# Optimization experiments

Measured on AMD Instinct MI355X. Metric: run time of the kernel, lower is better.

The kernel has to match this reference:

```python
import jax, jax.numpy as jnp
import numpy as np

N, R, A, F, T = 50000, 5, 8, 32, 32
TEMPLATE_RADIUS = 0.1


def _gaussian_prior_kernel():
    # Template vertices in polar coords -> cartesian; Gaussian interpolation prior.
    rho = np.linspace(TEMPLATE_RADIUS / R, TEMPLATE_RADIUS, R)
    theta = np.linspace(0.0, 2 * np.pi, A, endpoint=False)
    x = rho[:, None] * np.cos(theta)[None, :]  # [R, A]
    y = rho[:, None] * np.sin(theta)[None, :]
    pts = np.stack([x, y], axis=-1).reshape(R * A, 2)
    d2 = ((pts[:, None, :] - pts[None, :, :]) ** 2).sum(-1)
    sigma = TEMPLATE_RADIUS / R
    k = np.exp(-d2 / (2.0 * sigma ** 2)).astype(np.float32)
    return jnp.asarray(k.reshape(R, A, R, A))


def setup_inputs() -> dict:
    key = jax.random.key(0)
    k1, k2, k3, k4, k5, k6 = jax.random.split(key, 6)
    mesh_signal = jax.random.normal(k1, (N, F), dtype=jnp.float32)
    idx = jax.random.randint(k2, (N, R, A, 3), 0, N).astype(jnp.float32)
    w = jax.random.uniform(k3, (N, R, A, 3), dtype=jnp.float32)
    w = w / jnp.sum(w, axis=-1, keepdims=True)  # barycentric weights sum to 1
    bary_coordinates = jnp.stack([idx, w], axis=-1)  # [N,R,A,3,2]
    scale = 0.05
    W_self = jax.random.normal(k4, (T, 1, F), dtype=jnp.float32) * scale
    W_neighbor = jax.random.normal(k5, (T, R, A, F), dtype=jnp.float32) * scale
    bias = jax.random.normal(k6, (1, T), dtype=jnp.float32) * scale
    kernel = _gaussian_prior_kernel()
    return {"mesh_signal": mesh_signal, "bary_coordinates": bary_coordinates,
            "W_self": W_self, "W_neighbor": W_neighbor, "bias": bias, "kernel": kernel}


def reference(mesh_signal, bary_coordinates, W_self, W_neighbor, bias, kernel):
    # conv_center: [N, 1, T]
    conv_center = jnp.einsum('tef,kf->ket', W_self, mesh_signal)
    # Barycentric interpolation (gather + weighted sum over 3 triangle vertices)
    idx = bary_coordinates[..., 0].astype(jnp.int32)   # [N,R,A,3]
    w = bary_coordinates[..., 1]                        # [N,R,A,3]
    gathered = mesh_signal[idx]                         # [N,R,A,3,F]
    interp = jnp.sum(w[..., None] * gathered, axis=-2)  # [N,R,A,F]
    # Prior weighting: [R,A,R,A] x [N,R,A,F] -> [N,R,A,F]
    interp = jnp.einsum('raxy,kxyf->kraf', kernel, interp)
    # Rotations: torch.roll(interp, o, dims=2) contracted with W == roll(W, -o, axis=2) contracted with interp
    rotation_delta = 1
    orientations = range(0, A, rotation_delta)
    W_rot = jnp.stack([jnp.roll(W_neighbor, -o, axis=2) for o in orientations])  # [O,T,R,A,F]
    conv_neighbor = jnp.einsum('otraf,kraf->kot', W_rot, interp)  # [N,O,T]
    return jax.nn.relu(conv_center + conv_neighbor + bias)
```

## Files before the change

kernel.cpp:

```cpp
#include <hip/hip_runtime.h>
#include <hip/hip_fp16.h>

typedef unsigned short u16;
typedef unsigned int   u32;

#define N_MESH 50000
#define RA     40
#define F_     32
#define OT     256
#define KSELF  1280
#define KTOT   1312
#define NCH    41
#define GN     32
#define NBLK   1563
#define SECC   8
#define MESH16_BLOCKS 782
#define WEFF_BLOCKS   1312

using f32x4 = __attribute__((ext_vector_type(4))) float;
using f16x8 = __attribute__((ext_vector_type(8))) _Float16;

__device__ __align__(16) u16 g_bhi[NCH * 16 * 64 * 8];
__device__ __align__(16) u16 g_mesh16[N_MESH * F_];
__device__ int g_isf32;

__device__ __forceinline__ float bf2f(u16 u) {
    union { u32 i; float f; } v; v.i = ((u32)u) << 16; return v.f;
}
__device__ __forceinline__ u16 f2bf(float f) {
    union { float f; u32 i; } v; v.f = f; u32 u = v.i;
    return (u16)((u + 0x7FFFu + ((u >> 16) & 1u)) >> 16);
}
__device__ __forceinline__ float ld(const void* p, int i, int isf32) {
    return isf32 ? ((const float*)p)[i] : bf2f(((const u16*)p)[i]);
}

__global__ void detect_kernel(const void* mesh) {
    __shared__ int s_weird;
    if (threadIdx.x == 0) s_weird = 0;
    __syncthreads();
    const u16* p = (const u16*)mesh;
    int w = 0;
    for (int j = threadIdx.x * 16; j < threadIdx.x * 16 + 16; ++j) {
        float v = bf2f(p[j]);
        float a = v < 0.f ? -v : v;
        if (!(a <= 1.0e6f)) ++w;
        else if (a > 0.f && a < 1.0e-30f) ++w;
    }
    atomicAdd(&s_weird, w);
    __syncthreads();
    if (threadIdx.x == 0) g_isf32 = (s_weird > 100) ? 1 : 0;
}

__global__ void prep_kernel(const void* __restrict__ mesh,
                            const void* __restrict__ Wn,
                            const void* __restrict__ Wself,
                            const void* __restrict__ ker) {
    const int isf32 = g_isf32;
    if (blockIdx.x < MESH16_BLOCKS) {
        int i = blockIdx.x * 256 + threadIdx.x;
        if (i >= N_MESH * F_ / 8) return;
        union { uint4 v; _Float16 h[8]; } o;
        #pragma unroll
        for (int j = 0; j < 8; ++j)
            o.h[j] = (_Float16)ld(mesh, i * 8 + j, isf32);
        *((uint4*)g_mesh16 + i) = o.v;
    } else {
        int e = (blockIdx.x - MESH16_BLOCKS) * 256 + threadIdx.x;
        if (e >= OT * KTOT) return;
        int c = e / KTOT;
        int k = e - c * KTOT;
        int t = c & 31;
        float acc = 0.f;
        if (k < KSELF) {
            int xy = k >> 5, f = k & 31;
            int o = c >> 5;
            for (int ra = 0; ra < RA; ++ra) {
                int r = ra >> 3, a = ra & 7;
                int a2 = (a + o) & 7;
                acc += ld(ker, ra * RA + xy, isf32) *
                       ld(Wn, t * (5 * 8 * F_) + r * (8 * F_) + a2 * F_ + f, isf32);
            }
        } else {
            acc = ld(Wself, t * F_ + (k - KSELF), isf32);
        }
        int ch = k >> 5;
        int kg = (k >> 3) & 3;
        int el = k & 7;
        int nt = c >> 4, col = c & 15;
        size_t fi = ((size_t)(ch * 16 + nt) * 64 + (kg * 16 + col)) * 8 + el;
        union { _Float16 h; u16 u; } H;
        H.h = (_Float16)acc;
        g_bhi[fi] = H.u;
    }
}

__global__ __launch_bounds__(256, 4)
void ConvIntrinsic_17102559772776_kernel(const void* __restrict__ mesh,
                                         const void* __restrict__ bary,
                                         const void* __restrict__ bias,
                                         void* __restrict__ out) {
    __shared__ __align__(16) u16 Alds[SECC * 2 * 64 * 8];

    const int tid   = threadIdx.x;
    const int n0    = blockIdx.x * GN;
    const int isf32 = g_isf32;
    const int lane  = tid & 63;
    const int wv    = tid >> 6;
    const int clt   = tid >> 5;
    const int tn    = tid & 31;
    const int gn    = n0 + tn;
    const int rt1   = tn >> 4, lr = tn & 15;
    u16* const dst0 = Alds + ((size_t)(clt * 2 + rt1) * 64 + lr) * 8;

    f32x4 acc[2][4];
    #pragma unroll
    for (int rt = 0; rt < 2; ++rt)
        #pragma unroll
        for (int j = 0; j < 4; ++j) acc[rt][j] = (f32x4){0.f, 0.f, 0.f, 0.f};

    for (int sec = 0; sec < NCH; sec += SECC) {
        int nch = NCH - sec; if (nch > SECC) nch = SECC;

        if (clt < nch) {
            const int ch = sec + clt;
            if (gn >= N_MESH) {
                #pragma unroll
                for (int kg = 0; kg < 4; ++kg)
                    *(uint4*)(dst0 + kg * 128) = make_uint4(0, 0, 0, 0);
            } else if (ch < RA) {
                float fi0, w0, fi1, w1, fi2, w2;
                if (isf32) {
                    const float* bp = (const float*)bary + (size_t)gn * (RA * 6) + ch * 6;
                    fi0 = bp[0]; w0 = bp[1]; fi1 = bp[2]; w1 = bp[3]; fi2 = bp[4]; w2 = bp[5];
                } else {
                    const u16* bp = (const u16*)bary + (size_t)gn * (RA * 6) + ch * 6;
                    fi0 = bf2f(bp[0]); w0 = bf2f(bp[1]);
                    fi1 = bf2f(bp[2]); w1 = bf2f(bp[3]);
                    fi2 = bf2f(bp[4]); w2 = bf2f(bp[5]);
                }
                int i0 = (int)fi0, i1 = (int)fi1, i2 = (int)fi2;
                i0 = i0 < 0 ? 0 : (i0 > N_MESH - 1 ? N_MESH - 1 : i0);
                i1 = i1 < 0 ? 0 : (i1 > N_MESH - 1 ? N_MESH - 1 : i1);
                i2 = i2 < 0 ? 0 : (i2 > N_MESH - 1 ? N_MESH - 1 : i2);
                const uint4* m0 = (const uint4*)g_mesh16 + (size_t)i0 * 4;
                const uint4* m1 = (const uint4*)g_mesh16 + (size_t)i1 * 4;
                const uint4* m2 = (const uint4*)g_mesh16 + (size_t)i2 * 4;
                __half2 w0h = __float2half2_rn(w0);
                __half2 w1h = __float2half2_rn(w1);
                __half2 w2h = __float2half2_rn(w2);
                #pragma unroll
                for (int kg = 0; kg < 4; ++kg) {
                    union { uint4 v; __half2 h[4]; } x0, x1, x2, o;
                    x0.v = m0[kg]; x1.v = m1[kg]; x2.v = m2[kg];
                    #pragma unroll
                    for (int q = 0; q < 4; ++q)
                        o.h[q] = __hfma2(x0.h[q], w0h,
                                 __hfma2(x1.h[q], w1h, __hmul2(x2.h[q], w2h)));
                    *(uint4*)(dst0 + kg * 128) = o.v;
                }
            } else {
                const uint4* ms = (const uint4*)g_mesh16 + (size_t)gn * 4;
                #pragma unroll
                for (int kg = 0; kg < 4; ++kg)
                    *(uint4*)(dst0 + kg * 128) = ms[kg];
            }
        }
        __syncthreads();

        #pragma unroll 2
        for (int c = 0; c < nch; ++c) {
            int ch = sec + c;
            size_t bo = ((size_t)(ch * 16 + wv * 4) * 64 + lane) * 8;
            const f16x8* bh = (const f16x8*)&g_bhi[bo];
            f16x8 bhj[4];
            #pragma unroll
            for (int j = 0; j < 4; ++j) bhj[j] = bh[j * 64];
            #pragma unroll
            for (int rt = 0; rt < 2; ++rt) {
                f16x8 ah = *(const f16x8*)&Alds[((size_t)(c * 2 + rt) * 64 + lane) * 8];
                #pragma unroll
                for (int j = 0; j < 4; ++j)
                    acc[rt][j] = __builtin_amdgcn_mfma_f32_16x16x32_f16(ah, bhj[j], acc[rt][j], 0, 0, 0);
            }
        }
        __syncthreads();
    }

    const int col = lane & 15, rg = lane >> 4;
    #pragma unroll
    for (int j = 0; j < 4; ++j) {
        int c = (wv * 4 + j) * 16 + col;
        float bv = ld(bias, c & 31, isf32);
        #pragma unroll
        for (int rt = 0; rt < 2; ++rt) {
            #pragma unroll
            for (int r = 0; r < 4; ++r) {
                int row = n0 + rt * 16 + rg * 4 + r;
                if (row < N_MESH) {
                    float v = acc[rt][j][r] + bv;
                    v = v > 0.f ? v : 0.f;
                    size_t oi = (size_t)row * OT + c;
                    if (isf32) ((float*)out)[oi] = v;
                    else       ((u16*)out)[oi]   = f2bf(v);
                }
            }
        }
    }
}

extern "C" void kernel_launch(void* const* d_in, const int* in_sizes, int n_in,
                              void* d_out, int out_size, void* d_ws, size_t ws_size,
                              hipStream_t stream) {
    const void* mesh  = d_in[0];
    const void* bary  = d_in[1];
    const void* Wself = d_in[2];
    const void* Wn    = d_in[3];
    const void* bias  = d_in[4];
    const void* ker   = d_in[5];
    (void)in_sizes; (void)n_in; (void)out_size; (void)d_ws; (void)ws_size;

    detect_kernel<<<1, 256, 0, stream>>>(mesh);

    prep_kernel<<<MESH16_BLOCKS + WEFF_BLOCKS, 256, 0, stream>>>(mesh, Wn, Wself, ker);

    ConvIntrinsic_17102559772776_kernel<<<NBLK, 256, 0, stream>>>(mesh, bary, bias, d_out);
}
```

Baseline: 230.2 us.

## Build MFMA A-fragments directly in registers, dropping LDS staging and barriers

The main kernel no longer stages interpolated A tiles in shared memory with block barriers. Each wave now owns one 16-row tile and half of the output columns, and each lane gathers and interpolates its own 8-element A fragment straight into registers per chunk. The bary loads are also widened to 64-bit and 32-bit packed reads. In exchange, each interpolation is computed twice (once per column-group wave), more B fragments and accumulators are held per wave, and launch bounds are lowered to 3 blocks per SM to make room for the extra registers.

```diff
diff --git a/kernel.cpp b/kernel.cpp
--- a/kernel.cpp
+++ b/kernel.cpp
@@ -13,7 +13,6 @@
 #define NCH    41
 #define GN     32
 #define NBLK   1563
-#define SECC   8
 #define MESH16_BLOCKS 782
 #define WEFF_BLOCKS   1312
 
@@ -95,115 +94,90 @@
     }
 }
 
-__global__ __launch_bounds__(256, 4)
+__global__ __launch_bounds__(256, 3)
 void ConvIntrinsic_17102559772776_kernel(const void* __restrict__ mesh,
                                          const void* __restrict__ bary,
                                          const void* __restrict__ bias,
                                          void* __restrict__ out) {
-    __shared__ __align__(16) u16 Alds[SECC * 2 * 64 * 8];
-
     const int tid   = threadIdx.x;
     const int n0    = blockIdx.x * GN;
     const int isf32 = g_isf32;
     const int lane  = tid & 63;
-    const int wv    = tid >> 6;
-    const int clt   = tid >> 5;
-    const int tn    = tid & 31;
-    const int gn    = n0 + tn;
-    const int rt1   = tn >> 4, lr = tn & 15;
-    u16* const dst0 = Alds + ((size_t)(clt * 2 + rt1) * 64 + lr) * 8;
-
-    f32x4 acc[2][4];
+    const int w     = tid >> 6;
+    const int cg    = w & 1;
+    const int rt    = w >> 1;
+    const int arow  = lane & 15;
+    const int p     = lane >> 4;
+    const int gn    = n0 + rt * 16 + arow;
+    const bool valid = (gn < N_MESH);
+
+    f32x4 acc[8];
     #pragma unroll
-    for (int rt = 0; rt < 2; ++rt)
-        #pragma unroll
-        for (int j = 0; j < 4; ++j) acc[rt][j] = (f32x4){0.f, 0.f, 0.f, 0.f};
-
-    for (int sec = 0; sec < NCH; sec += SECC) {
-        int nch = NCH - sec; if (nch > SECC) nch = SECC;
-
-        if (clt < nch) {
-            const int ch = sec + clt;
-            if (gn >= N_MESH) {
-                #pragma unroll
-                for (int kg = 0; kg < 4; ++kg)
-                    *(uint4*)(dst0 + kg * 128) = make_uint4(0, 0, 0, 0);
-            } else if (ch < RA) {
-                float fi0, w0, fi1, w1, fi2, w2;
-                if (isf32) {
-                    const float* bp = (const float*)bary + (size_t)gn * (RA * 6) + ch * 6;
-                    fi0 = bp[0]; w0 = bp[1]; fi1 = bp[2]; w1 = bp[3]; fi2 = bp[4]; w2 = bp[5];
-                } else {
-                    const u16* bp = (const u16*)bary + (size_t)gn * (RA * 6) + ch * 6;
-                    fi0 = bf2f(bp[0]); w0 = bf2f(bp[1]);
-                    fi1 = bf2f(bp[2]); w1 = bf2f(bp[3]);
-                    fi2 = bf2f(bp[4]); w2 = bf2f(bp[5]);
-                }
-                int i0 = (int)fi0, i1 = (int)fi1, i2 = (int)fi2;
-                i0 = i0 < 0 ? 0 : (i0 > N_MESH - 1 ? N_MESH - 1 : i0);
-                i1 = i1 < 0 ? 0 : (i1 > N_MESH - 1 ? N_MESH - 1 : i1);
-                i2 = i2 < 0 ? 0 : (i2 > N_MESH - 1 ? N_MESH - 1 : i2);
-                const uint4* m0 = (const uint4*)g_mesh16 + (size_t)i0 * 4;
-                const uint4* m1 = (const uint4*)g_mesh16 + (size_t)i1 * 4;
-                const uint4* m2 = (const uint4*)g_mesh16 + (size_t)i2 * 4;
-                __half2 w0h = __float2half2_rn(w0);
-                __half2 w1h = __float2half2_rn(w1);
-                __half2 w2h = __float2half2_rn(w2);
-                #pragma unroll
-                for (int kg = 0; kg < 4; ++kg) {
-                    union { uint4 v; __half2 h[4]; } x0, x1, x2, o;
-                    x0.v = m0[kg]; x1.v = m1[kg]; x2.v = m2[kg];
-                    #pragma unroll
-                    for (int q = 0; q < 4; ++q)
-                        o.h[q] = __hfma2(x0.h[q], w0h,
-                                 __hfma2(x1.h[q], w1h, __hmul2(x2.h[q], w2h)));
-                    *(uint4*)(dst0 + kg * 128) = o.v;
-                }
+    for (int j = 0; j < 8; ++j) acc[j] = (f32x4){0.f, 0.f, 0.f, 0.f};
+
+    #pragma unroll 2
+    for (int ch = 0; ch < NCH; ++ch) {
+        const f16x8* bh = (const f16x8*)&g_bhi[((size_t)(ch * 16 + cg * 8) * 64 + lane) * 8];
+        f16x8 bhj[8];
+        #pragma unroll
+        for (int j = 0; j < 8; ++j) bhj[j] = bh[j * 64];
+
+        union { uint4 v; __half2 h[4]; f16x8 f; } ah;
+        if (!valid) {
+            ah.v = make_uint4(0, 0, 0, 0);
+        } else if (ch < RA) {
+            float fi0, w0, fi1, w1, fi2, w2;
+            if (isf32) {
+                const uint2* bp = (const uint2*)((const float*)bary + (size_t)gn * (RA * 6) + ch * 6);
+                uint2 pa = bp[0], pb = bp[1], pc = bp[2];
+                fi0 = __uint_as_float(pa.x); w0 = __uint_as_float(pa.y);
+                fi1 = __uint_as_float(pb.x); w1 = __uint_as_float(pb.y);
+                fi2 = __uint_as_float(pc.x); w2 = __uint_as_float(pc.y);
             } else {
-                const uint4* ms = (const uint4*)g_mesh16 + (size_t)gn * 4;
-                #pragma unroll
-                for (int kg = 0; kg < 4; ++kg)
-                    *(uint4*)(dst0 + kg * 128) = ms[kg];
+                const u32* bp = (const u32*)((const u16*)bary + (size_t)gn * (RA * 6) + ch * 6);
+                u32 d0 = bp[0], d1 = bp[1], d2 = bp[2];
+                fi0 = bf2f((u16)(d0 & 0xffffu)); w0 = bf2f((u16)(d0 >> 16));
+                fi1 = bf2f((u16)(d1 & 0xffffu)); w1 = bf2f((u16)(d1 >> 16));
+                fi2 = bf2f((u16)(d2 & 0xffffu)); w2 = bf2f((u16)(d2 >> 16));
             }
+            int i0 = (int)fi0, i1 = (int)fi1, i2 = (int)fi2;
+            i0 = i0 < 0 ? 0 : (i0 > N_MESH - 1 ? N_MESH - 1 : i0);
+            i1 = i1 < 0 ? 0 : (i1 > N_MESH - 1 ? N_MESH - 1 : i1);
+            i2 = i2 < 0 ? 0 : (i2 > N_MESH - 1 ? N_MESH - 1 : i2);
+            union { uint4 v; __half2 h[4]; } x0, x1, x2;
+            x0.v = *((const uint4*)(g_mesh16 + (size_t)i0 * F_) + p);
+            x1.v = *((const uint4*)(g_mesh16 + (size_t)i1 * F_) + p);
+            x2.v = *((const uint4*)(g_mesh16 + (size_t)i2 * F_) + p);
+            __half2 w0h = __float2half2_rn(w0);
+            __half2 w1h = __float2half2_rn(w1);
+            __half2 w2h = __float2half2_rn(w2);
+            #pragma unroll
+            for (int q = 0; q < 4; ++q)
+                ah.h[q] = __hfma2(x0.h[q], w0h,
+                          __hfma2(x1.h[q], w1h, __hmul2(x2.h[q], w2h)));
+        } else {
+            ah.v = *((const uint4*)(g_mesh16 + (size_t)gn * F_) + p);
         }
-        __syncthreads();
-
-        #pragma unroll 2
-        for (int c = 0; c < nch; ++c) {
-            int ch = sec + c;
-            size_t bo = ((size_t)(ch * 16 + wv * 4) * 64 + lane) * 8;
-            const f16x8* bh = (const f16x8*)&g_bhi[bo];
-            f16x8 bhj[4];
-            #pragma unroll
-            for (int j = 0; j < 4; ++j) bhj[j] = bh[j * 64];
-            #pragma unroll
-            for (int rt = 0; rt < 2; ++rt) {
-                f16x8 ah = *(const f16x8*)&Alds[((size_t)(c * 2 + rt) * 64 + lane) * 8];
-                #pragma unroll
-                for (int j = 0; j < 4; ++j)
-                    acc[rt][j] = __builtin_amdgcn_mfma_f32_16x16x32_f16(ah, bhj[j], acc[rt][j], 0, 0, 0);
-            }
-        }
-        __syncthreads();
+
+        #pragma unroll
+        for (int j = 0; j < 8; ++j)
+            acc[j] = __builtin_amdgcn_mfma_f32_16x16x32_f16(ah.f, bhj[j], acc[j], 0, 0, 0);
     }
 
     const int col = lane & 15, rg = lane >> 4;
     #pragma unroll
-    for (int j = 0; j < 4; ++j) {
-        int c = (wv * 4 + j) * 16 + col;
+    for (int j = 0; j < 8; ++j) {
+        int c = (cg * 8 + j) * 16 + col;
         float bv = ld(bias, c & 31, isf32);
         #pragma unroll
-        for (int rt = 0; rt < 2; ++rt) {
-            #pragma unroll
-            for (int r = 0; r < 4; ++r) {
-                int row = n0 + rt * 16 + rg * 4 + r;
-                if (row < N_MESH) {
-                    float v = acc[rt][j][r] + bv;
-                    v = v > 0.f ? v : 0.f;
-                    size_t oi = (size_t)row * OT + c;
-                    if (isf32) ((float*)out)[oi] = v;
-                    else       ((u16*)out)[oi]   = f2bf(v);
-                }
+        for (int r = 0; r < 4; ++r) {
+            int row = n0 + rt * 16 + rg * 4 + r;
+            if (row < N_MESH) {
+                float v = acc[j][r] + bv;
+                v = v > 0.f ? v : 0.f;
+                size_t oi = (size_t)row * OT + c;
+                if (isf32) ((float*)out)[oi] = v;
+                else       ((u16*)out)[oi]   = f2bf(v);
             }
         }
     }
```

New measurement: 322.2 us. 40.0% more time.
